# Kernel tuning notes

Hardware: AMD Instinct MI355X
Metric: run time of the kernel (lower is better)

## Reference

```python
import jax, jax.numpy as jnp
import numpy as np

STEPS = 1  # GNConvolution recurrent update steps

N_ATOMS, N_BONDS, N_GRAPHS = 8192, 131072, 16
ATOM_DIM, BOND_DIM, STATE_DIM = 32, 32, 32


def setup_inputs() -> dict:
    key = jax.random.key(0)
    ks = jax.random.split(key, 12)
    d, bd, sd = ATOM_DIM, BOND_DIM, STATE_DIM
    return {
        "atom_features": jax.random.normal(ks[0], (N_ATOMS, d), jnp.float32),
        "bond_features": jax.random.normal(ks[1], (N_BONDS, bd), jnp.float32),
        "state_attrs": jax.random.normal(ks[2], (N_GRAPHS, sd), jnp.float32),
        # stacked params for the 3 convs (query, key, value)
        "W_edge": jax.random.normal(ks[3], (3, bd + sd, d * d), jnp.float32) * 0.05,
        "b_edge": jnp.zeros((3, d * d), jnp.float32),
        "W_x": jax.random.normal(ks[4], (3, d, 3 * d), jnp.float32) * 0.1,
        "W_h": jax.random.normal(ks[5], (3, d, 3 * d), jnp.float32) * 0.1,
        "b_x": jnp.zeros((3, 3 * d), jnp.float32),
        "b_h": jnp.zeros((3, 3 * d), jnp.float32),
        "pair_indices": jax.random.randint(ks[6], (N_BONDS, 2), 0, N_ATOMS, jnp.int64),
        "atom_graph_indices": jnp.sort(jax.random.randint(ks[7], (N_ATOMS,), 0, N_GRAPHS, jnp.int64)),
        "bond_graph_indices": jnp.sort(jax.random.randint(ks[8], (N_BONDS,), 0, N_GRAPHS, jnp.int64)),
    }


def _gn_conv(atom, bond, state, pair, bond_g, We, be, Wx, Wh, bx, bh):
    """MatDGL GNConvolution: edge-conditioned message passing + GRU update."""
    n_atoms, d = atom.shape
    # edge network: concat(bond, state gathered per bond) -> d x d filter per edge
    edge_in = jnp.concatenate([bond, state[bond_g]], axis=-1)        # [E, bd+sd]
    filt = (edge_in @ We + be).reshape(-1, d, d)                     # [E, d, d]
    neigh = atom[pair[:, 1]]                                         # [E, d]
    msg = jnp.einsum('eij,ej->ei', filt, neigh)                      # [E, d]
    agg = jax.ops.segment_sum(msg, pair[:, 0], num_segments=n_atoms) # [N, d]
    # GRU cell update (reset_after=True, keras default)
    h = atom
    for _ in range(STEPS):
        mx = agg @ Wx + bx
        mh = h @ Wh + bh
        xz, xr, xh = jnp.split(mx, 3, axis=-1)
        hz, hr, hh = jnp.split(mh, 3, axis=-1)
        z = jax.nn.sigmoid(xz + hz)
        r = jax.nn.sigmoid(xr + hr)
        hc = jnp.tanh(xh + r * hh)
        h = z * h + (1.0 - z) * hc
    return h


def reference(atom_features, bond_features, state_attrs, W_edge, b_edge,
              W_x, W_h, b_x, b_h, pair_indices, atom_graph_indices,
              bond_graph_indices):
    d = atom_features.shape[-1]
    conv = jax.vmap(_gn_conv,
                    in_axes=(None, None, None, None, None, 0, 0, 0, 0, 0, 0))
    qkv = conv(atom_features, bond_features, state_attrs, pair_indices,
               bond_graph_indices, W_edge, b_edge, W_x, W_h, b_x, b_h)
    q, k, v = qkv[0], qkv[1], qkv[2]                                 # [N, d] each
    scores = (q @ k.T) / jnp.asarray(d, q.dtype) ** 0.5              # [N, N]
    attn = jax.nn.softmax(scores, axis=-1)
    return attn @ v                                                  # [N, d]
```

## Files before the change

kernel.cpp:

```cpp
#include <hip/hip_runtime.h>
#include <hip/hip_bf16.h>
#include <math.h>

#define NA 8192
#define NB 131072
#define NG 16
#define NSHARD 16

#define OFF_BH   0u
#define OFF_VB   49152u
#define OFF_AGG  73728u
#define OFF_QH   860160u
#define OFF_QL   991232u
#define OFF_KH   1122304u
#define OFF_KL   1253376u
#define OFF_VTH  1384448u
#define OFF_VTL  1515520u
#define OFF_NUM  1646592u
#define OFF_DEN  5840896u

typedef __attribute__((ext_vector_type(8))) short short8;
typedef __attribute__((ext_vector_type(4))) float f4;
typedef __attribute__((ext_vector_type(2))) float f2;
typedef __attribute__((ext_vector_type(2))) unsigned int uint2v;

__device__ inline unsigned short bfb(float x) {
    __hip_bfloat16 b = __float2bfloat16(x);
    return reinterpret_cast<unsigned short&>(b);
}
__device__ inline float bf2f(unsigned short u) {
    unsigned int x = ((unsigned int)u) << 16;
    return __uint_as_float(x);
}
__device__ inline unsigned int pk2(float x, float y) {
    __hip_bfloat162 t = __float22bfloat162_rn(make_float2(x, y));
    union { __hip_bfloat162 b; unsigned int u; } cv;
    cv.b = t;
    return cv.u;
}

__global__ __launch_bounds__(256) void prep_bh(const float* __restrict__ We,
                                               unsigned short* __restrict__ Bh)
{
    int idx = blockIdx.x * 256 + threadIdx.x;
    int hc = idx >> 8;
    int n4 = (idx & 255) * 4;
    const float4 v = *(const float4*)(We + ((size_t)((hc >> 5) * 64 + (hc & 31))) * 1024 + n4);
    unsigned short* d = Bh + (size_t)hc * 1024 + n4;
    d[0] = bfb(v.x); d[1] = bfb(v.y); d[2] = bfb(v.z); d[3] = bfb(v.w);
}

__global__ __launch_bounds__(256) void prep_v(const float* __restrict__ state,
    const float* __restrict__ We, const float* __restrict__ be,
    unsigned short* __restrict__ Vb)
{
    int h = blockIdx.x >> 4, g = blockIdx.x & 15;
    const float* st = state + g * 32;
    const float* W  = We + ((size_t)h * 64 + 32) * 1024;
    const float* bb = be + (size_t)h * 1024;
    int n = threadIdx.x * 4;
    float4 acc = *(const float4*)(bb + n);
    for (int c = 0; c < 32; ++c) {
        float s = st[c];
        const float4 w = *(const float4*)(W + c * 1024 + n);
        acc.x += s * w.x; acc.y += s * w.y; acc.z += s * w.z; acc.w += s * w.w;
    }
    unsigned short* d = Vb + ((size_t)h * 16 + g) * 1024 + n;
    d[0] = bfb(acc.x); d[1] = bfb(acc.y); d[2] = bfb(acc.z); d[3] = bfb(acc.w);
}

__global__ __launch_bounds__(256) void msg_mfma(
    const float* __restrict__ atom, const float* __restrict__ bond,
    const unsigned short* __restrict__ Bh, const unsigned short* __restrict__ Vb,
    const int* __restrict__ pair, const int* __restrict__ bg,
    float* __restrict__ agg)
{
    __shared__ float bl[128 * 36];
    __shared__ int gmm[2];
    const int tid = threadIdx.x;
    const int h  = blockIdx.y;
    const int e0 = blockIdx.x * 128;
    for (int x = tid; x < 1024; x += 256) {
        int e = x >> 3, c4 = (x & 7) << 2;
        float4 v = *(const float4*)(bond + (size_t)(e0 + e) * 32 + c4);
        float* d = &bl[e * 36 + c4];
        d[0] = v.x; d[1] = v.y; d[2] = v.z; d[3] = v.w;
    }
    if (tid == 0) { gmm[0] = bg[e0]; gmm[1] = bg[e0 + 127]; }

    const int wave = tid >> 6, lane = tid & 63;
    const int ln = lane & 15, quad = lane >> 4;
    const int em0 = e0 + wave * 32 + ln;
    const int em1 = em0 + 16;
    const int src0 = pair[2 * em0 + 1], src1 = pair[2 * em1 + 1];
    const int gv0 = bg[em0], gv1 = bg[em1];
    f2 n0p[4], n1p[4];
    {
        const float* p0 = atom + (size_t)src0 * 32 + quad * 8;
        const float* p1 = atom + (size_t)src1 * 32 + quad * 8;
        float4 a = *(const float4*)p0, b = *(const float4*)(p0 + 4);
        n0p[0] = f2{a.x, a.y}; n0p[1] = f2{a.z, a.w};
        n0p[2] = f2{b.x, b.y}; n0p[3] = f2{b.z, b.w};
        float4 c = *(const float4*)p1, d = *(const float4*)(p1 + 4);
        n1p[0] = f2{c.x, c.y}; n1p[1] = f2{c.z, c.w};
        n1p[2] = f2{d.x, d.y}; n1p[3] = f2{d.z, d.w};
    }
    __syncthreads();
    f4 acc00 = {0,0,0,0}, acc01 = {0,0,0,0}, acc10 = {0,0,0,0}, acc11 = {0,0,0,0};
    const unsigned short* bp = Bh + (size_t)h * 32 * 1024 + ln * 32 + quad * 8;
    const int bo0 = (wave * 32 + ln) * 36;
    const int bo1 = bo0 + 16 * 36;
    #pragma unroll 2
    for (int c4 = 0; c4 < 32; c4 += 4) {
        f4 cv0 = *(const f4*)&bl[bo0 + c4];
        f4 cv1 = *(const f4*)&bl[bo1 + c4];
        #pragma unroll
        for (int u = 0; u < 4; ++u) {
            const unsigned short* bpc = bp + (c4 + u) * 1024;
            short8 b0 = *(const short8*)bpc;
            short8 b1 = *(const short8*)(bpc + 512);
            float c0 = cv0[u], c1 = cv1[u];
            union { unsigned int u4[4]; short8 s; } A0, A1;
            #pragma unroll
            for (int q2 = 0; q2 < 4; ++q2) {
                f2 p0 = c0 * n0p[q2];
                f2 p1 = c1 * n1p[q2];
                A0.u4[q2] = pk2(p0.x, p0.y);
                A1.u4[q2] = pk2(p1.x, p1.y);
            }
            acc00 = __builtin_amdgcn_mfma_f32_16x16x32_bf16(A0.s, b0, acc00, 0, 0, 0);
            acc01 = __builtin_amdgcn_mfma_f32_16x16x32_bf16(A0.s, b1, acc01, 0, 0, 0);
            acc10 = __builtin_amdgcn_mfma_f32_16x16x32_bf16(A1.s, b0, acc10, 0, 0, 0);
            acc11 = __builtin_amdgcn_mfma_f32_16x16x32_bf16(A1.s, b1, acc11, 0, 0, 0);
        }
    }
    union { unsigned int u4[4]; short8 s; } NB0, NB1;
    #pragma unroll
    for (int q2 = 0; q2 < 4; ++q2) {
        NB0.u4[q2] = pk2(n0p[q2].x, n0p[q2].y);
        NB1.u4[q2] = pk2(n1p[q2].x, n1p[q2].y);
    }
    const short8 zz = {0,0,0,0,0,0,0,0};
    const int gmin = gmm[0], gmax = gmm[1];
    for (int g = gmin; g <= gmax; ++g) {
        const unsigned short* vp = Vb + ((size_t)h * 16 + g) * 1024 + ln * 32 + quad * 8;
        short8 b0 = *(const short8*)vp;
        short8 b1 = *(const short8*)(vp + 512);
        short8 a0 = (gv0 == g) ? NB0.s : zz;
        short8 a1 = (gv1 == g) ? NB1.s : zz;
        acc00 = __builtin_amdgcn_mfma_f32_16x16x32_bf16(a0, b0, acc00, 0, 0, 0);
        acc01 = __builtin_amdgcn_mfma_f32_16x16x32_bf16(a0, b1, acc01, 0, 0, 0);
        acc10 = __builtin_amdgcn_mfma_f32_16x16x32_bf16(a1, b0, acc10, 0, 0, 0);
        acc11 = __builtin_amdgcn_mfma_f32_16x16x32_bf16(a1, b1, acc11, 0, 0, 0);
    }
    #pragma unroll
    for (int r = 0; r < 4; ++r) {
        int eA = e0 + wave * 32 + quad * 4 + r;
        int eB = eA + 16;
        int aA = pair[2 * eA], aB = pair[2 * eB];
        float* dA = agg + ((size_t)h * NA + aA) * 32;
        float* dB = agg + ((size_t)h * NA + aB) * 32;
        atomicAdd(dA + ln,      acc00[r]);
        atomicAdd(dA + 16 + ln, acc01[r]);
        atomicAdd(dB + ln,      acc10[r]);
        atomicAdd(dB + 16 + ln, acc11[r]);
    }
}

__global__ __launch_bounds__(256) void gru_kernel(
    const float* __restrict__ atom, const float* __restrict__ agg,
    const float* __restrict__ Wx, const float* __restrict__ Wh,
    const float* __restrict__ bx, const float* __restrict__ bh,
    unsigned short* __restrict__ Qh, unsigned short* __restrict__ Ql,
    unsigned short* __restrict__ Kh, unsigned short* __restrict__ Kl,
    unsigned short* __restrict__ Vth, unsigned short* __restrict__ Vtl)
{
    __shared__ float ag[8][33], at[8][33], hb[8][33];
    const int tid = threadIdx.x;
    const int r = tid >> 5, i = tid & 31;
    const int ha = blockIdx.x * 8 + r;
    const int h = ha >> 13;
    const int a = ha & 8191;
    ag[r][i] = agg[(size_t)ha * 32 + i];
    at[r][i] = atom[(size_t)a * 32 + i];
    __syncthreads();
    const float* wx = Wx + (size_t)h * 32 * 96;
    const float* wh = Wh + (size_t)h * 32 * 96;
    float x0 = bx[h*96 + i], x1 = bx[h*96 + 32 + i], x2 = bx[h*96 + 64 + i];
    float g0 = bh[h*96 + i], g1 = bh[h*96 + 32 + i], g2 = bh[h*96 + 64 + i];
    #pragma unroll 4
    for (int c = 0; c < 32; ++c) {
        float av = ag[r][c], hv = at[r][c];
        x0 += av * wx[c*96 + i]; x1 += av * wx[c*96 + 32 + i]; x2 += av * wx[c*96 + 64 + i];
        g0 += hv * wh[c*96 + i]; g1 += hv * wh[c*96 + 32 + i]; g2 += hv * wh[c*96 + 64 + i];
    }
    float z  = 1.f / (1.f + __expf(-(x0 + g0)));
    float rr = 1.f / (1.f + __expf(-(x1 + g1)));
    float hc = tanhf(x2 + rr * g2);
    float hn = z * at[r][i] + (1.f - z) * hc;
    if (h == 0) {
        float x = hn * 0.1767766952966369f;
        unsigned short hi = bfb(x);
        Qh[(size_t)a * 32 + i] = hi;
        Ql[(size_t)a * 32 + i] = bfb(x - bf2f(hi));
    } else if (h == 1) {
        unsigned short hi = bfb(hn);
        Kh[(size_t)a * 32 + i] = hi;
        Kl[(size_t)a * 32 + i] = bfb(hn - bf2f(hi));
    } else {
        hb[r][i] = hn;
        __syncthreads();
        const int a0 = blockIdx.x * 8 - 2 * NA;
        const int i2 = tid >> 3, a2 = tid & 7;
        float v = hb[a2][i2];
        unsigned short hi = bfb(v);
        Vth[(size_t)i2 * NA + a0 + a2] = hi;
        Vtl[(size_t)i2 * NA + a0 + a2] = bfb(v - bf2f(hi));
    }
}

__global__ __launch_bounds__(256) void attn_mfma(
    const unsigned short* __restrict__ Qh, const unsigned short* __restrict__ Ql,
    const unsigned short* __restrict__ Kh, const unsigned short* __restrict__ Kl,
    const unsigned short* __restrict__ Vth, const unsigned short* __restrict__ Vtl,
    float* __restrict__ num, float* __restrict__ den)
{
    __shared__ unsigned short pb[4][32 * 40];
    const int tid = threadIdx.x;
    const int wave = tid >> 6, lane = tid & 63;
    const int ln = lane & 15, quad = lane >> 4;
    const int sh = blockIdx.y;
    const int q0 = blockIdx.x * 128 + wave * 32;

    short8 qh0 = *(const short8*)(Qh + (size_t)(q0 + ln) * 32 + quad * 8);
    short8 ql0 = *(const short8*)(Ql + (size_t)(q0 + ln) * 32 + quad * 8);
    short8 qh1 = *(const short8*)(Qh + (size_t)(q0 + 16 + ln) * 32 + quad * 8);
    short8 ql1 = *(const short8*)(Ql + (size_t)(q0 + 16 + ln) * 32 + quad * 8);

    f4 a00 = {0,0,0,0}, a01 = {0,0,0,0}, a10 = {0,0,0,0}, a11 = {0,0,0,0};
    float l0 = 0.f, l1 = 0.f;
    unsigned short* pw = &pb[wave][0];

    const int kbeg = sh * (NA / NSHARD);
    for (int k0 = kbeg; k0 < kbeg + NA / NSHARD; k0 += 32) {
        const size_t ko0 = (size_t)(k0 + ln) * 32 + quad * 8;
        const size_t ko1 = (size_t)(k0 + 16 + ln) * 32 + quad * 8;
        short8 kh0 = *(const short8*)(Kh + ko0);
        short8 kh1 = *(const short8*)(Kh + ko1);
        short8 kl0 = *(const short8*)(Kl + ko0);
        short8 kl1 = *(const short8*)(Kl + ko1);

        f4 s00 = {0,0,0,0}, s01 = {0,0,0,0}, s10 = {0,0,0,0}, s11 = {0,0,0,0};
        s00 = __builtin_amdgcn_mfma_f32_16x16x32_bf16(kl0, qh0, s00, 0, 0, 0);
        s00 = __builtin_amdgcn_mfma_f32_16x16x32_bf16(kh0, ql0, s00, 0, 0, 0);
        s00 = __builtin_amdgcn_mfma_f32_16x16x32_bf16(kh0, qh0, s00, 0, 0, 0);
        s01 = __builtin_amdgcn_mfma_f32_16x16x32_bf16(kl0, qh1, s01, 0, 0, 0);
        s01 = __builtin_amdgcn_mfma_f32_16x16x32_bf16(kh0, ql1, s01, 0, 0, 0);
        s01 = __builtin_amdgcn_mfma_f32_16x16x32_bf16(kh0, qh1, s01, 0, 0, 0);
        s10 = __builtin_amdgcn_mfma_f32_16x16x32_bf16(kl1, qh0, s10, 0, 0, 0);
        s10 = __builtin_amdgcn_mfma_f32_16x16x32_bf16(kh1, ql0, s10, 0, 0, 0);
        s10 = __builtin_amdgcn_mfma_f32_16x16x32_bf16(kh1, qh0, s10, 0, 0, 0);
        s11 = __builtin_amdgcn_mfma_f32_16x16x32_bf16(kl1, qh1, s11, 0, 0, 0);
        s11 = __builtin_amdgcn_mfma_f32_16x16x32_bf16(kh1, ql1, s11, 0, 0, 0);
        s11 = __builtin_amdgcn_mfma_f32_16x16x32_bf16(kh1, qh1, s11, 0, 0, 0);

        {
            float e0 = __expf(s00[0]-64.f), e1 = __expf(s00[1]-64.f),
                  e2 = __expf(s00[2]-64.f), e3 = __expf(s00[3]-64.f);
            l0 += (e0+e1)+(e2+e3);
            *(uint2v*)&pw[ln*40 + quad*4] = uint2v{pk2(e0,e1), pk2(e2,e3)};
            e0 = __expf(s10[0]-64.f); e1 = __expf(s10[1]-64.f);
            e2 = __expf(s10[2]-64.f); e3 = __expf(s10[3]-64.f);
            l0 += (e0+e1)+(e2+e3);
            *(uint2v*)&pw[ln*40 + 16 + quad*4] = uint2v{pk2(e0,e1), pk2(e2,e3)};
            e0 = __expf(s01[0]-64.f); e1 = __expf(s01[1]-64.f);
            e2 = __expf(s01[2]-64.f); e3 = __expf(s01[3]-64.f);
            l1 += (e0+e1)+(e2+e3);
            *(uint2v*)&pw[(16+ln)*40 + quad*4] = uint2v{pk2(e0,e1), pk2(e2,e3)};
            e0 = __expf(s11[0]-64.f); e1 = __expf(s11[1]-64.f);
            e2 = __expf(s11[2]-64.f); e3 = __expf(s11[3]-64.f);
            l1 += (e0+e1)+(e2+e3);
            *(uint2v*)&pw[(16+ln)*40 + 16 + quad*4] = uint2v{pk2(e0,e1), pk2(e2,e3)};
        }
        short8 pa0 = *(const short8*)&pw[ln*40 + quad*8];
        short8 pa1 = *(const short8*)&pw[(16+ln)*40 + quad*8];

        const size_t vo0 = (size_t)ln * NA + k0 + quad * 8;
        const size_t vo1 = (size_t)(16 + ln) * NA + k0 + quad * 8;
        short8 vh0 = *(const short8*)(Vth + vo0);
        short8 vh1 = *(const short8*)(Vth + vo1);
        short8 vl0 = *(const short8*)(Vtl + vo0);
        short8 vl1 = *(const short8*)(Vtl + vo1);

        a00 = __builtin_amdgcn_mfma_f32_16x16x32_bf16(pa0, vl0, a00, 0, 0, 0);
        a00 = __builtin_amdgcn_mfma_f32_16x16x32_bf16(pa0, vh0, a00, 0, 0, 0);
        a01 = __builtin_amdgcn_mfma_f32_16x16x32_bf16(pa0, vl1, a01, 0, 0, 0);
        a01 = __builtin_amdgcn_mfma_f32_16x16x32_bf16(pa0, vh1, a01, 0, 0, 0);
        a10 = __builtin_amdgcn_mfma_f32_16x16x32_bf16(pa1, vl0, a10, 0, 0, 0);
        a10 = __builtin_amdgcn_mfma_f32_16x16x32_bf16(pa1, vh0, a10, 0, 0, 0);
        a11 = __builtin_amdgcn_mfma_f32_16x16x32_bf16(pa1, vl1, a11, 0, 0, 0);
        a11 = __builtin_amdgcn_mfma_f32_16x16x32_bf16(pa1, vh1, a11, 0, 0, 0);
    }
    l0 += __shfl_xor(l0, 16); l0 += __shfl_xor(l0, 32);
    l1 += __shfl_xor(l1, 16); l1 += __shfl_xor(l1, 32);

    #pragma unroll
    for (int r = 0; r < 4; ++r) {
        const int row0 = q0 + quad * 4 + r;
        float* np = num + ((size_t)sh * NA + row0) * 32;
        np[ln] = a00[r]; np[16 + ln] = a01[r];
        float* nq = num + ((size_t)sh * NA + row0 + 16) * 32;
        nq[ln] = a10[r]; nq[16 + ln] = a11[r];
    }
    if (quad == 0) {
        den[(size_t)sh * NA + q0 + ln]      = l0;
        den[(size_t)sh * NA + q0 + 16 + ln] = l1;
    }
}

__global__ __launch_bounds__(256) void merge_kernel(const float* __restrict__ num,
                                                    const float* __restrict__ den,
                                                    float* __restrict__ out)
{
    const int tid = threadIdx.x;
    const int r = tid >> 5, c = tid & 31;
    const int q = blockIdx.x * 8 + r;
    float ds = 0.f, ns = 0.f;
    #pragma unroll
    for (int sh = 0; sh < NSHARD; ++sh) {
        ns += num[((size_t)sh * NA + q) * 32 + c];
        ds += den[(size_t)sh * NA + q];
    }
    out[(size_t)q * 32 + c] = ns / ds;
}

extern "C" void kernel_launch(void* const* d_in, const int* in_sizes, int n_in,
                              void* d_out, int out_size, void* d_ws, size_t ws_size,
                              hipStream_t stream)
{
    const float* atom  = (const float*)d_in[0];
    const float* bond  = (const float*)d_in[1];
    const float* state = (const float*)d_in[2];
    const float* We    = (const float*)d_in[3];
    const float* be    = (const float*)d_in[4];
    const float* Wx    = (const float*)d_in[5];
    const float* Wh    = (const float*)d_in[6];
    const float* bx    = (const float*)d_in[7];
    const float* bh    = (const float*)d_in[8];
    const int*   pair  = (const int*)d_in[9];
    const int*   bg    = (const int*)d_in[11];
    float* ws = (float*)d_ws;
    unsigned short* Bh  = (unsigned short*)(ws + OFF_BH);
    unsigned short* Vb  = (unsigned short*)(ws + OFF_VB);
    float* agg  = ws + OFF_AGG;
    unsigned short* Qh  = (unsigned short*)(ws + OFF_QH);
    unsigned short* Ql  = (unsigned short*)(ws + OFF_QL);
    unsigned short* Kh  = (unsigned short*)(ws + OFF_KH);
    unsigned short* Kl  = (unsigned short*)(ws + OFF_KL);
    unsigned short* Vth = (unsigned short*)(ws + OFF_VTH);
    unsigned short* Vtl = (unsigned short*)(ws + OFF_VTL);
    float* num = ws + OFF_NUM;
    float* den = ws + OFF_DEN;
    float* out = (float*)d_out;

    hipMemsetAsync(agg, 0, (size_t)3 * NA * 32 * sizeof(float), stream);
    prep_bh<<<96, 256, 0, stream>>>(We, Bh);
    prep_v<<<48, 256, 0, stream>>>(state, We, be, Vb);
    msg_mfma<<<dim3(NB / 128, 3), 256, 0, stream>>>(atom, bond, Bh, Vb, pair, bg, agg);
    gru_kernel<<<3 * NA / 8, 256, 0, stream>>>(atom, agg, Wx, Wh, bx, bh,
                                               Qh, Ql, Kh, Kl, Vth, Vtl);
    attn_mfma<<<dim3(NA / 128, NSHARD), 256, 0, stream>>>(Qh, Ql, Kh, Kl, Vth, Vtl, num, den);
    merge_kernel<<<NA / 8, 256, 0, stream>>>(num, den, out);
}
```

Before: 247.2 us.

## Pass softmax probabilities via ds_bpermute instead of LDS and transpose PV MFMA

Drops the per-wave LDS staging buffer for the exponentiated score tile in the attention kernel. Probabilities are now packed to bf16 and redistributed across lanes with ds_bpermute so they can be fed directly as the B operand of a transposed P·V MFMA. As a result the partial numerators come out column-major, so the store layout and the merge kernel's reads change to match. This removes LDS write/read round trips and their waits, at the cost of more cross-lane permute instructions and selects per iteration.

After: 254.9 us. 3.1% more time.

```diff
diff --git a/kernel.cpp b/kernel.cpp
--- a/kernel.cpp
+++ b/kernel.cpp
@@ -22,7 +22,6 @@
 typedef __attribute__((ext_vector_type(8))) short short8;
 typedef __attribute__((ext_vector_type(4))) float f4;
 typedef __attribute__((ext_vector_type(2))) float f2;
-typedef __attribute__((ext_vector_type(2))) unsigned int uint2v;
 
 __device__ inline unsigned short bfb(float x) {
     __hip_bfloat16 b = __float2bfloat16(x);
@@ -37,6 +36,9 @@
     union { __hip_bfloat162 b; unsigned int u; } cv;
     cv.b = t;
     return cv.u;
+}
+__device__ inline unsigned int bperm(int lane_byte, unsigned int v) {
+    return (unsigned int)__builtin_amdgcn_ds_bpermute(lane_byte, (int)v);
 }
 
 __global__ __launch_bounds__(256) void prep_bh(const float* __restrict__ We,
@@ -225,7 +227,6 @@
     const unsigned short* __restrict__ Vth, const unsigned short* __restrict__ Vtl,
     float* __restrict__ num, float* __restrict__ den)
 {
-    __shared__ unsigned short pb[4][32 * 40];
     const int tid = threadIdx.x;
     const int wave = tid >> 6, lane = tid & 63;
     const int ln = lane & 15, quad = lane >> 4;
@@ -237,9 +238,12 @@
     short8 qh1 = *(const short8*)(Qh + (size_t)(q0 + 16 + ln) * 32 + quad * 8);
     short8 ql1 = *(const short8*)(Ql + (size_t)(q0 + 16 + ln) * 32 + quad * 8);
 
-    f4 a00 = {0,0,0,0}, a01 = {0,0,0,0}, a10 = {0,0,0,0}, a11 = {0,0,0,0};
+    f4 o00 = {0,0,0,0}, o01 = {0,0,0,0}, o10 = {0,0,0,0}, o11 = {0,0,0,0};
     float l0 = 0.f, l1 = 0.f;
-    unsigned short* pw = &pb[wave][0];
+
+    const int laneA = (ln + ((quad & 1) << 5)) << 2;
+    const int laneB = laneA + (16 << 2);
+    const bool hiK = (quad >= 2);
 
     const int kbeg = sh * (NA / NSHARD);
     for (int k0 = kbeg; k0 < kbeg + NA / NSHARD; k0 += 32) {
@@ -264,26 +268,37 @@
         s11 = __builtin_amdgcn_mfma_f32_16x16x32_bf16(kh1, ql1, s11, 0, 0, 0);
         s11 = __builtin_amdgcn_mfma_f32_16x16x32_bf16(kh1, qh1, s11, 0, 0, 0);
 
+        float e00_0 = __expf(s00[0]-64.f), e00_1 = __expf(s00[1]-64.f),
+              e00_2 = __expf(s00[2]-64.f), e00_3 = __expf(s00[3]-64.f);
+        float e10_0 = __expf(s10[0]-64.f), e10_1 = __expf(s10[1]-64.f),
+              e10_2 = __expf(s10[2]-64.f), e10_3 = __expf(s10[3]-64.f);
+        float e01_0 = __expf(s01[0]-64.f), e01_1 = __expf(s01[1]-64.f),
+              e01_2 = __expf(s01[2]-64.f), e01_3 = __expf(s01[3]-64.f);
+        float e11_0 = __expf(s11[0]-64.f), e11_1 = __expf(s11[1]-64.f),
+              e11_2 = __expf(s11[2]-64.f), e11_3 = __expf(s11[3]-64.f);
+        l0 += ((e00_0+e00_1)+(e00_2+e00_3)) + ((e10_0+e10_1)+(e10_2+e10_3));
+        l1 += ((e01_0+e01_1)+(e01_2+e01_3)) + ((e11_0+e11_1)+(e11_2+e11_3));
+
+        unsigned int t0u0a = pk2(e00_0, e00_1), t0u1a = pk2(e00_2, e00_3);
+        unsigned int t0u0b = pk2(e10_0, e10_1), t0u1b = pk2(e10_2, e10_3);
+        unsigned int t1u0a = pk2(e01_0, e01_1), t1u1a = pk2(e01_2, e01_3);
+        unsigned int t1u0b = pk2(e11_0, e11_1), t1u1b = pk2(e11_2, e11_3);
+
+        union { unsigned int u[4]; short8 s; } P0, P1;
         {
-            float e0 = __expf(s00[0]-64.f), e1 = __expf(s00[1]-64.f),
-                  e2 = __expf(s00[2]-64.f), e3 = __expf(s00[3]-64.f);
-            l0 += (e0+e1)+(e2+e3);
-            *(uint2v*)&pw[ln*40 + quad*4] = uint2v{pk2(e0,e1), pk2(e2,e3)};
-            e0 = __expf(s10[0]-64.f); e1 = __expf(s10[1]-64.f);
-            e2 = __expf(s10[2]-64.f); e3 = __expf(s10[3]-64.f);
-            l0 += (e0+e1)+(e2+e3);
-            *(uint2v*)&pw[ln*40 + 16 + quad*4] = uint2v{pk2(e0,e1), pk2(e2,e3)};
-            e0 = __expf(s01[0]-64.f); e1 = __expf(s01[1]-64.f);
-            e2 = __expf(s01[2]-64.f); e3 = __expf(s01[3]-64.f);
-            l1 += (e0+e1)+(e2+e3);
-            *(uint2v*)&pw[(16+ln)*40 + quad*4] = uint2v{pk2(e0,e1), pk2(e2,e3)};
-            e0 = __expf(s11[0]-64.f); e1 = __expf(s11[1]-64.f);
-            e2 = __expf(s11[2]-64.f); e3 = __expf(s11[3]-64.f);
-            l1 += (e0+e1)+(e2+e3);
-            *(uint2v*)&pw[(16+ln)*40 + 16 + quad*4] = uint2v{pk2(e0,e1), pk2(e2,e3)};
+            unsigned int a0 = bperm(laneA, t0u0a), b0 = bperm(laneA, t0u0b);
+            unsigned int a1 = bperm(laneA, t0u1a), b1 = bperm(laneA, t0u1b);
+            unsigned int a2 = bperm(laneB, t0u0a), b2 = bperm(laneB, t0u0b);
+            unsigned int a3 = bperm(laneB, t0u1a), b3 = bperm(laneB, t0u1b);
+            P0.u[0] = hiK ? b0 : a0; P0.u[1] = hiK ? b1 : a1;
+            P0.u[2] = hiK ? b2 : a2; P0.u[3] = hiK ? b3 : a3;
+            a0 = bperm(laneA, t1u0a); b0 = bperm(laneA, t1u0b);
+            a1 = bperm(laneA, t1u1a); b1 = bperm(laneA, t1u1b);
+            a2 = bperm(laneB, t1u0a); b2 = bperm(laneB, t1u0b);
+            a3 = bperm(laneB, t1u1a); b3 = bperm(laneB, t1u1b);
+            P1.u[0] = hiK ? b0 : a0; P1.u[1] = hiK ? b1 : a1;
+            P1.u[2] = hiK ? b2 : a2; P1.u[3] = hiK ? b3 : a3;
         }
-        short8 pa0 = *(const short8*)&pw[ln*40 + quad*8];
-        short8 pa1 = *(const short8*)&pw[(16+ln)*40 + quad*8];
 
         const size_t vo0 = (size_t)ln * NA + k0 + quad * 8;
         const size_t vo1 = (size_t)(16 + ln) * NA + k0 + quad * 8;
@@ -292,25 +307,24 @@
         short8 vl0 = *(const short8*)(Vtl + vo0);
         short8 vl1 = *(const short8*)(Vtl + vo1);
 
-        a00 = __builtin_amdgcn_mfma_f32_16x16x32_bf16(pa0, vl0, a00, 0, 0, 0);
-        a00 = __builtin_amdgcn_mfma_f32_16x16x32_bf16(pa0, vh0, a00, 0, 0, 0);
-        a01 = __builtin_amdgcn_mfma_f32_16x16x32_bf16(pa0, vl1, a01, 0, 0, 0);
-        a01 = __builtin_amdgcn_mfma_f32_16x16x32_bf16(pa0, vh1, a01, 0, 0, 0);
-        a10 = __builtin_amdgcn_mfma_f32_16x16x32_bf16(pa1, vl0, a10, 0, 0, 0);
-        a10 = __builtin_amdgcn_mfma_f32_16x16x32_bf16(pa1, vh0, a10, 0, 0, 0);
-        a11 = __builtin_amdgcn_mfma_f32_16x16x32_bf16(pa1, vl1, a11, 0, 0, 0);
-        a11 = __builtin_amdgcn_mfma_f32_16x16x32_bf16(pa1, vh1, a11, 0, 0, 0);
+        o00 = __builtin_amdgcn_mfma_f32_16x16x32_bf16(vl0, P0.s, o00, 0, 0, 0);
+        o00 = __builtin_amdgcn_mfma_f32_16x16x32_bf16(vh0, P0.s, o00, 0, 0, 0);
+        o01 = __builtin_amdgcn_mfma_f32_16x16x32_bf16(vl0, P1.s, o01, 0, 0, 0);
+        o01 = __builtin_amdgcn_mfma_f32_16x16x32_bf16(vh0, P1.s, o01, 0, 0, 0);
+        o10 = __builtin_amdgcn_mfma_f32_16x16x32_bf16(vl1, P0.s, o10, 0, 0, 0);
+        o10 = __builtin_amdgcn_mfma_f32_16x16x32_bf16(vh1, P0.s, o10, 0, 0, 0);
+        o11 = __builtin_amdgcn_mfma_f32_16x16x32_bf16(vl1, P1.s, o11, 0, 0, 0);
+        o11 = __builtin_amdgcn_mfma_f32_16x16x32_bf16(vh1, P1.s, o11, 0, 0, 0);
     }
     l0 += __shfl_xor(l0, 16); l0 += __shfl_xor(l0, 32);
     l1 += __shfl_xor(l1, 16); l1 += __shfl_xor(l1, 32);
 
     #pragma unroll
     for (int r = 0; r < 4; ++r) {
-        const int row0 = q0 + quad * 4 + r;
-        float* np = num + ((size_t)sh * NA + row0) * 32;
-        np[ln] = a00[r]; np[16 + ln] = a01[r];
-        float* nq = num + ((size_t)sh * NA + row0 + 16) * 32;
-        nq[ln] = a10[r]; nq[16 + ln] = a11[r];
+        float* n0 = num + ((size_t)sh * 32 + quad * 4 + r) * NA + q0;
+        n0[ln] = o00[r]; n0[16 + ln] = o01[r];
+        float* n1 = num + ((size_t)sh * 32 + 16 + quad * 4 + r) * NA + q0;
+        n1[ln] = o10[r]; n1[16 + ln] = o11[r];
     }
     if (quad == 0) {
         den[(size_t)sh * NA + q0 + ln]      = l0;
@@ -323,12 +337,12 @@
                                                     float* __restrict__ out)
 {
     const int tid = threadIdx.x;
-    const int r = tid >> 5, c = tid & 31;
-    const int q = blockIdx.x * 8 + r;
+    const int c = tid >> 3, qi = tid & 7;
+    const int q = blockIdx.x * 8 + qi;
     float ds = 0.f, ns = 0.f;
     #pragma unroll
     for (int sh = 0; sh < NSHARD; ++sh) {
-        ns += num[((size_t)sh * NA + q) * 32 + c];
+        ns += num[((size_t)sh * 32 + c) * NA + q];
         ds += den[(size_t)sh * NA + q];
     }
     out[(size_t)q * 32 + c] = ns / ds;
```

## Replace atomic scatter-add aggregation with CSR-sorted gather of bf16 messages

Applied to the files above, without the earlier changes.

Builds a CSR index of bonds by destination atom (count, scan, scatter permutation) and has the message kernel write per-edge bf16 messages instead of float atomics into agg. The GRU kernel then gathers and sums each atom's messages through the permutation, which removes the float atomic contention and the memset of agg. It also merges the two weight-prep kernels into one launch that also does the counting. The cost is extra launches, a single-block scan, a 25 MB message buffer written and read back, irregular gathers in the GRU, and bf16 rounding of each message before summation.

Measured after the change: 263.8 us. +6.7%, slower.

```diff
diff --git a/kernel.cpp b/kernel.cpp
--- a/kernel.cpp
+++ b/kernel.cpp
@@ -9,15 +9,19 @@
 
 #define OFF_BH   0u
 #define OFF_VB   49152u
-#define OFF_AGG  73728u
-#define OFF_QH   860160u
-#define OFF_QL   991232u
-#define OFF_KH   1122304u
-#define OFF_KL   1253376u
-#define OFF_VTH  1384448u
-#define OFF_VTL  1515520u
-#define OFF_NUM  1646592u
-#define OFF_DEN  5840896u
+#define OFF_CNT  73728u
+#define OFF_CUR  81920u
+#define OFF_RP   90112u
+#define OFF_PERM 98304u
+#define OFF_QH   229376u
+#define OFF_QL   360448u
+#define OFF_KH   491520u
+#define OFF_KL   622592u
+#define OFF_VTH  753664u
+#define OFF_VTL  884736u
+#define OFF_MSG  1015808u
+#define OFF_NUM  1015808u
+#define OFF_DEN  7307264u
 
 typedef __attribute__((ext_vector_type(8))) short short8;
 typedef __attribute__((ext_vector_type(4))) float f4;
@@ -39,41 +43,81 @@
     return cv.u;
 }
 
-__global__ __launch_bounds__(256) void prep_bh(const float* __restrict__ We,
-                                               unsigned short* __restrict__ Bh)
-{
-    int idx = blockIdx.x * 256 + threadIdx.x;
-    int hc = idx >> 8;
-    int n4 = (idx & 255) * 4;
-    const float4 v = *(const float4*)(We + ((size_t)((hc >> 5) * 64 + (hc & 31))) * 1024 + n4);
-    unsigned short* d = Bh + (size_t)hc * 1024 + n4;
-    d[0] = bfb(v.x); d[1] = bfb(v.y); d[2] = bfb(v.z); d[3] = bfb(v.w);
-}
-
-__global__ __launch_bounds__(256) void prep_v(const float* __restrict__ state,
-    const float* __restrict__ We, const float* __restrict__ be,
-    unsigned short* __restrict__ Vb)
-{
-    int h = blockIdx.x >> 4, g = blockIdx.x & 15;
-    const float* st = state + g * 32;
-    const float* W  = We + ((size_t)h * 64 + 32) * 1024;
-    const float* bb = be + (size_t)h * 1024;
-    int n = threadIdx.x * 4;
-    float4 acc = *(const float4*)(bb + n);
-    for (int c = 0; c < 32; ++c) {
-        float s = st[c];
-        const float4 w = *(const float4*)(W + c * 1024 + n);
-        acc.x += s * w.x; acc.y += s * w.y; acc.z += s * w.z; acc.w += s * w.w;
-    }
-    unsigned short* d = Vb + ((size_t)h * 16 + g) * 1024 + n;
-    d[0] = bfb(acc.x); d[1] = bfb(acc.y); d[2] = bfb(acc.z); d[3] = bfb(acc.w);
+__global__ __launch_bounds__(256) void prep_all(
+    const float* __restrict__ We, const float* __restrict__ state,
+    const float* __restrict__ be, const int* __restrict__ pair,
+    unsigned short* __restrict__ Bh, unsigned short* __restrict__ Vb,
+    int* __restrict__ cnt)
+{
+    const int bid = blockIdx.x, tid = threadIdx.x;
+    const int e = bid * 256 + tid;
+    atomicAdd(&cnt[pair[2 * e]], 1);
+    if (bid < 96) {
+        int idx = bid * 256 + tid;
+        int hc = idx >> 8;
+        int n4 = (idx & 255) * 4;
+        const float4 v = *(const float4*)(We + ((size_t)((hc >> 5) * 64 + (hc & 31))) * 1024 + n4);
+        unsigned short* d = Bh + (size_t)hc * 1024 + n4;
+        d[0] = bfb(v.x); d[1] = bfb(v.y); d[2] = bfb(v.z); d[3] = bfb(v.w);
+    } else if (bid < 144) {
+        int b2 = bid - 96;
+        int h = b2 >> 4, g = b2 & 15;
+        const float* st = state + g * 32;
+        const float* W  = We + ((size_t)h * 64 + 32) * 1024;
+        const float* bb = be + (size_t)h * 1024;
+        int n = tid * 4;
+        float4 acc = *(const float4*)(bb + n);
+        for (int c = 0; c < 32; ++c) {
+            float s = st[c];
+            const float4 w = *(const float4*)(W + c * 1024 + n);
+            acc.x += s * w.x; acc.y += s * w.y; acc.z += s * w.z; acc.w += s * w.w;
+        }
+        unsigned short* d = Vb + ((size_t)h * 16 + g) * 1024 + n;
+        d[0] = bfb(acc.x); d[1] = bfb(acc.y); d[2] = bfb(acc.z); d[3] = bfb(acc.w);
+    }
+}
+
+__global__ __launch_bounds__(256) void scan_kernel(const int* __restrict__ cnt,
+                                                   int* __restrict__ cur,
+                                                   int* __restrict__ rp)
+{
+    __shared__ int part[256];
+    const int t = threadIdx.x;
+    const int base = t * 32;
+    int loc[32];
+    int s = 0;
+    #pragma unroll
+    for (int k = 0; k < 32; ++k) { loc[k] = cnt[base + k]; s += loc[k]; }
+    part[t] = s;
+    __syncthreads();
+    for (int off = 1; off < 256; off <<= 1) {
+        int add = (t >= off) ? part[t - off] : 0;
+        __syncthreads();
+        part[t] += add;
+        __syncthreads();
+    }
+    int excl = part[t] - s;
+    #pragma unroll
+    for (int k = 0; k < 32; ++k) {
+        cur[base + k] = excl; rp[base + k] = excl; excl += loc[k];
+    }
+}
+
+__global__ __launch_bounds__(256) void scatter_kernel(const int* __restrict__ pair,
+                                                      int* __restrict__ cur,
+                                                      int* __restrict__ perm)
+{
+    const int e = blockIdx.x * 256 + threadIdx.x;
+    const int d = pair[2 * e];
+    const int p = atomicAdd(&cur[d], 1);
+    perm[p] = e;
 }
 
 __global__ __launch_bounds__(256) void msg_mfma(
     const float* __restrict__ atom, const float* __restrict__ bond,
     const unsigned short* __restrict__ Bh, const unsigned short* __restrict__ Vb,
     const int* __restrict__ pair, const int* __restrict__ bg,
-    float* __restrict__ agg)
+    unsigned short* __restrict__ msgbuf)
 {
     __shared__ float bl[128 * 36];
     __shared__ int gmm[2];
@@ -157,18 +201,18 @@
     for (int r = 0; r < 4; ++r) {
         int eA = e0 + wave * 32 + quad * 4 + r;
         int eB = eA + 16;
-        int aA = pair[2 * eA], aB = pair[2 * eB];
-        float* dA = agg + ((size_t)h * NA + aA) * 32;
-        float* dB = agg + ((size_t)h * NA + aB) * 32;
-        atomicAdd(dA + ln,      acc00[r]);
-        atomicAdd(dA + 16 + ln, acc01[r]);
-        atomicAdd(dB + ln,      acc10[r]);
-        atomicAdd(dB + 16 + ln, acc11[r]);
+        unsigned short* dA = msgbuf + ((size_t)h * NB + eA) * 32;
+        unsigned short* dB = msgbuf + ((size_t)h * NB + eB) * 32;
+        dA[ln]      = bfb(acc00[r]);
+        dA[16 + ln] = bfb(acc01[r]);
+        dB[ln]      = bfb(acc10[r]);
+        dB[16 + ln] = bfb(acc11[r]);
     }
 }
 
 __global__ __launch_bounds__(256) void gru_kernel(
-    const float* __restrict__ atom, const float* __restrict__ agg,
+    const float* __restrict__ atom, const unsigned short* __restrict__ msgbuf,
+    const int* __restrict__ rp, const int* __restrict__ perm,
     const float* __restrict__ Wx, const float* __restrict__ Wh,
     const float* __restrict__ bx, const float* __restrict__ bh,
     unsigned short* __restrict__ Qh, unsigned short* __restrict__ Ql,
@@ -181,7 +225,17 @@
     const int ha = blockIdx.x * 8 + r;
     const int h = ha >> 13;
     const int a = ha & 8191;
-    ag[r][i] = agg[(size_t)ha * 32 + i];
+    {
+        const int beg = rp[a];
+        const int end = (a == NA - 1) ? NB : rp[a + 1];
+        const unsigned short* mb = msgbuf + (size_t)h * NB * 32 + i;
+        float av = 0.f;
+        for (int x = beg; x < end; ++x) {
+            int e = perm[x];
+            av += bf2f(mb[(size_t)e * 32]);
+        }
+        ag[r][i] = av;
+    }
     at[r][i] = atom[(size_t)a * 32 + i];
     __syncthreads();
     const float* wx = Wx + (size_t)h * 32 * 96;
@@ -352,22 +406,27 @@
     float* ws = (float*)d_ws;
     unsigned short* Bh  = (unsigned short*)(ws + OFF_BH);
     unsigned short* Vb  = (unsigned short*)(ws + OFF_VB);
-    float* agg  = ws + OFF_AGG;
+    int* cnt  = (int*)(ws + OFF_CNT);
+    int* cur  = (int*)(ws + OFF_CUR);
+    int* rp   = (int*)(ws + OFF_RP);
+    int* perm = (int*)(ws + OFF_PERM);
     unsigned short* Qh  = (unsigned short*)(ws + OFF_QH);
     unsigned short* Ql  = (unsigned short*)(ws + OFF_QL);
     unsigned short* Kh  = (unsigned short*)(ws + OFF_KH);
     unsigned short* Kl  = (unsigned short*)(ws + OFF_KL);
     unsigned short* Vth = (unsigned short*)(ws + OFF_VTH);
     unsigned short* Vtl = (unsigned short*)(ws + OFF_VTL);
+    unsigned short* msgbuf = (unsigned short*)(ws + OFF_MSG);
     float* num = ws + OFF_NUM;
     float* den = ws + OFF_DEN;
     float* out = (float*)d_out;
 
-    hipMemsetAsync(agg, 0, (size_t)3 * NA * 32 * sizeof(float), stream);
-    prep_bh<<<96, 256, 0, stream>>>(We, Bh);
-    prep_v<<<48, 256, 0, stream>>>(state, We, be, Vb);
-    msg_mfma<<<dim3(NB / 128, 3), 256, 0, stream>>>(atom, bond, Bh, Vb, pair, bg, agg);
-    gru_kernel<<<3 * NA / 8, 256, 0, stream>>>(atom, agg, Wx, Wh, bx, bh,
+    hipMemsetAsync(cnt, 0, NA * sizeof(int), stream);
+    prep_all<<<512, 256, 0, stream>>>(We, state, be, pair, Bh, Vb, cnt);
+    scan_kernel<<<1, 256, 0, stream>>>(cnt, cur, rp);
+    scatter_kernel<<<512, 256, 0, stream>>>(pair, cur, perm);
+    msg_mfma<<<dim3(NB / 128, 3), 256, 0, stream>>>(atom, bond, Bh, Vb, pair, bg, msgbuf);
+    gru_kernel<<<3 * NA / 8, 256, 0, stream>>>(atom, msgbuf, rp, perm, Wx, Wh, bx, bh,
                                                Qh, Ql, Kh, Kl, Vth, Vtl);
     attn_mfma<<<dim3(NA / 128, NSHARD), 256, 0, stream>>>(Qh, Ql, Kh, Kl, Vth, Vtl, num, den);
     merge_kernel<<<NA / 8, 256, 0, stream>>>(num, den, out);
```
